# Kernel optimization log

Hardware: AMD Instinct MI355X
Metric: run time of the kernel (lower is better)

## Reference

```python
import jax, jax.numpy as jnp
import numpy as np

EMB_DIM = 256
ATTN_DIM = 64
N_HEADS = 2
B = 32768
K = 16


def setup_inputs() -> dict:
    key = jax.random.key(0)
    ks = jax.random.split(key, 8)
    center_emb = jax.random.normal(ks[0], (B, EMB_DIM), dtype=jnp.float32)
    neigh_embs = jax.random.normal(ks[1], (B, K, EMB_DIM), dtype=jnp.float32)
    neigh_weights = jax.random.uniform(ks[2], (B, K), dtype=jnp.float32)
    valid_mask = jax.random.randint(ks[3], (B,), 0, 2) > 0  # bool [B]
    # parameters (torch nn.Linear convention: y = x @ W.T)
    sq = 1.0 / np.sqrt(EMB_DIM)
    W_q = jax.random.uniform(ks[4], (N_HEADS, ATTN_DIM, EMB_DIM), minval=-sq, maxval=sq, dtype=jnp.float32)
    W_k = jax.random.uniform(ks[5], (N_HEADS, ATTN_DIM, EMB_DIM), minval=-sq, maxval=sq, dtype=jnp.float32)
    so = 1.0 / np.sqrt(EMB_DIM * N_HEADS)
    W_out = jax.random.uniform(ks[6], (EMB_DIM, EMB_DIM * N_HEADS), minval=-so, maxval=so, dtype=jnp.float32)
    b_out = jax.random.uniform(ks[7], (EMB_DIM,), minval=-so, maxval=so, dtype=jnp.float32)
    return {
        "center_emb": center_emb,
        "neigh_embs": neigh_embs,
        "neigh_weights": neigh_weights,
        "valid_mask": valid_mask,
        "W_q": W_q,
        "W_k": W_k,
        "W_out": W_out,
        "b_out": b_out,
    }


def reference(center_emb, neigh_embs, neigh_weights, valid_mask, W_q, W_k, W_out, b_out):
    # q: [B, H, A]; k: [B, H, K, A] (all heads vectorized)
    q = jnp.einsum("bd,had->bha", center_emb, W_q)
    k = jnp.einsum("bkd,had->bhka", neigh_embs, W_k)
    scores = jnp.einsum("bha,bhka->bhk", q, k) / jnp.sqrt(jnp.float32(ATTN_DIM))
    attn = jax.nn.softmax(scores, axis=-1) * neigh_weights[:, None, :]  # [B,H,K]
    attn = attn / (jnp.sum(attn, axis=-1, keepdims=True) + 1e-8)
    # dropout is identity in eval mode
    ctx = jnp.einsum("bhk,bkd->bhd", attn, neigh_embs)  # [B,H,D]
    multi_ctx = ctx.reshape(ctx.shape[0], -1)  # concat heads -> [B, H*D]
    out = multi_ctx @ W_out.T + b_out
    return jnp.where(valid_mask[:, None], out, center_emb)
```

## Files before the change

### kernel.cpp

```cpp
#include <hip/hip_runtime.h>
#include <hip/hip_bf16.h>

typedef unsigned short ushort_t;
typedef unsigned int uint32;

typedef __attribute__((ext_vector_type(8))) short bf16x8;
typedef __attribute__((ext_vector_type(4))) float f32x4;

__device__ __forceinline__ ushort_t f2bf(float f) {
    uint32 u = __float_as_uint(f);
    u += 0x7FFFu + ((u >> 16) & 1u);
    return (ushort_t)(u >> 16);
}
__device__ __forceinline__ float bf2f(ushort_t b) {
    return __uint_as_float(((uint32)b) << 16);
}

__global__ __launch_bounds__(256) void prep_kernel(
        const float* __restrict__ Wq, const float* __restrict__ Wk,
        const float* __restrict__ Wout,
        ushort_t* __restrict__ Mcomb, ushort_t* __restrict__ WoutB) {
    int idx = blockIdx.x * 256 + threadIdx.x;
    int n = idx >> 8;
    int e = idx & 255;
    int h = n >> 8;
    int d = n & 255;
    const float* wk = Wk + (h << 14);
    const float* wq = Wq + (h << 14);
    float acc = 0.f;
#pragma unroll 8
    for (int a = 0; a < 64; ++a) {
        acc += wk[(a << 8) + d] * wq[(a << 8) + e];
    }
    Mcomb[idx] = f2bf(acc * 0.125f);
    WoutB[idx] = f2bf(Wout[idx]);
}

#define LDT 72

__global__ __launch_bounds__(256) void gemm_qk(
        const float* __restrict__ A, const ushort_t* __restrict__ Bw,
        ushort_t* __restrict__ C) {
    __shared__ ushort_t As[64 * LDT];
    __shared__ ushort_t Bs[128 * LDT];
    const int t = threadIdx.x;
    const int m0 = blockIdx.x * 64;
    const int n0 = blockIdx.y * 128;
    const int lane = t & 63;
    const int w = t >> 6;
    const int wm = (w & 1) * 32;
    const int wn = (w >> 1) * 64;

    f32x4 zero = {0.f, 0.f, 0.f, 0.f};
    f32x4 acc[2][4];
#pragma unroll
    for (int i = 0; i < 2; ++i)
#pragma unroll
        for (int j = 0; j < 4; ++j) acc[i][j] = zero;

    for (int kc = 0; kc < 256; kc += 64) {
        __syncthreads();
#pragma unroll
        for (int i = 0; i < 4; ++i) {
            int f = i * 1024 + t * 4;
            int r = f >> 6;
            int c = f & 63;
            float4 v = *reinterpret_cast<const float4*>(&A[(size_t)(m0 + r) * 256 + kc + c]);
            ushort_t p[4] = {f2bf(v.x), f2bf(v.y), f2bf(v.z), f2bf(v.w)};
            *reinterpret_cast<uint2*>(&As[r * LDT + c]) = *reinterpret_cast<uint2*>(p);
        }
#pragma unroll
        for (int i = 0; i < 4; ++i) {
            int f = i * 2048 + t * 8;
            int r = f >> 6;
            int c = f & 63;
            uint4 v = *reinterpret_cast<const uint4*>(&Bw[(size_t)(n0 + r) * 256 + kc + c]);
            *reinterpret_cast<uint4*>(&Bs[r * LDT + c]) = v;
        }
        __syncthreads();
#pragma unroll
        for (int s = 0; s < 2; ++s) {
            int kb = s * 32 + (lane >> 4) * 8;
            bf16x8 af[2], bfr[4];
#pragma unroll
            for (int i = 0; i < 2; ++i)
                af[i] = *reinterpret_cast<const bf16x8*>(&As[(wm + i * 16 + (lane & 15)) * LDT + kb]);
#pragma unroll
            for (int j = 0; j < 4; ++j)
                bfr[j] = *reinterpret_cast<const bf16x8*>(&Bs[(wn + j * 16 + (lane & 15)) * LDT + kb]);
#pragma unroll
            for (int i = 0; i < 2; ++i)
#pragma unroll
                for (int j = 0; j < 4; ++j)
                    acc[i][j] = __builtin_amdgcn_mfma_f32_16x16x32_bf16(af[i], bfr[j], acc[i][j], 0, 0, 0);
        }
    }
    const int cn = lane & 15;
    const int r4 = (lane >> 4) * 4;
#pragma unroll
    for (int i = 0; i < 2; ++i)
#pragma unroll
        for (int j = 0; j < 4; ++j)
#pragma unroll
            for (int r = 0; r < 4; ++r) {
                int m = m0 + wm + i * 16 + r4 + r;
                int n = n0 + wn + j * 16 + cn;
                C[(size_t)m * 512 + n] = f2bf(acc[i][j][r]);
            }
}

#define XSS 264

__global__ __launch_bounds__(256) void attn_kernel(
        const float* __restrict__ neigh, const float* __restrict__ wts,
        const ushort_t* __restrict__ qk, ushort_t* __restrict__ ctx) {
    __shared__ ushort_t xs[4][16 * XSS];
    __shared__ float qs[4][512];
    __shared__ float at[4][32];
    const int t = threadIdx.x;
    const int w = t >> 6;
    const int lane = t & 63;
    const size_t b = (size_t)blockIdx.x * 4 + w;

    const float* xg = neigh + b * 4096;
#pragma unroll
    for (int k = 0; k < 16; ++k) {
        float4 v = *reinterpret_cast<const float4*>(&xg[k * 256 + lane * 4]);
        ushort_t p[4] = {f2bf(v.x), f2bf(v.y), f2bf(v.z), f2bf(v.w)};
        *reinterpret_cast<uint2*>(&xs[w][k * XSS + lane * 4]) = *reinterpret_cast<uint2*>(p);
    }
    {
        uint4 v = *reinterpret_cast<const uint4*>(&qk[b * 512 + lane * 8]);
        const ushort_t* xu = reinterpret_cast<const ushort_t*>(&v);
        float4 q0 = {bf2f(xu[0]), bf2f(xu[1]), bf2f(xu[2]), bf2f(xu[3])};
        float4 q1 = {bf2f(xu[4]), bf2f(xu[5]), bf2f(xu[6]), bf2f(xu[7])};
        *reinterpret_cast<float4*>(&qs[w][lane * 8]) = q0;
        *reinterpret_cast<float4*>(&qs[w][lane * 8 + 4]) = q1;
    }
    __syncthreads();

    const int p = lane & 31;
    const int half = lane >> 5;
    const int h = p >> 4;
    const int kn = p & 15;
    const ushort_t* xrow = &xs[w][kn * XSS + half * 128];
    const float* qrow = &qs[w][h * 256 + half * 128];
    float sc = 0.f;
#pragma unroll
    for (int j = 0; j < 16; ++j) {
        uint4 xv = *reinterpret_cast<const uint4*>(xrow + j * 8);
        const ushort_t* xu = reinterpret_cast<const ushort_t*>(&xv);
        float4 q0 = *reinterpret_cast<const float4*>(qrow + j * 8);
        float4 q1 = *reinterpret_cast<const float4*>(qrow + j * 8 + 4);
        sc += bf2f(xu[0]) * q0.x;
        sc += bf2f(xu[1]) * q0.y;
        sc += bf2f(xu[2]) * q0.z;
        sc += bf2f(xu[3]) * q0.w;
        sc += bf2f(xu[4]) * q1.x;
        sc += bf2f(xu[5]) * q1.y;
        sc += bf2f(xu[6]) * q1.z;
        sc += bf2f(xu[7]) * q1.w;
    }
    sc += __shfl_xor(sc, 32);

    float mx = sc;
#pragma unroll
    for (int m = 1; m < 16; m <<= 1) mx = fmaxf(mx, __shfl_xor(mx, m));
    float e = __expf(sc - mx);
    float se = e;
#pragma unroll
    for (int m = 1; m < 16; m <<= 1) se += __shfl_xor(se, m);
    float wv = wts[b * 16 + kn];
    float num = (e / se) * wv;
    float den = num;
#pragma unroll
    for (int m = 1; m < 16; m <<= 1) den += __shfl_xor(den, m);
    float attn = num / (den + 1e-8f);
    if (half == 0) at[w][h * 16 + kn] = attn;
    __syncthreads();

    const int h2 = lane >> 5;
    const int db = (lane & 31) * 8;
    float acc[8];
#pragma unroll
    for (int i = 0; i < 8; ++i) acc[i] = 0.f;
#pragma unroll
    for (int kk = 0; kk < 16; ++kk) {
        float a = at[w][h2 * 16 + kk];
        uint4 xv = *reinterpret_cast<const uint4*>(&xs[w][kk * XSS + db]);
        const ushort_t* xu = reinterpret_cast<const ushort_t*>(&xv);
#pragma unroll
        for (int i = 0; i < 8; ++i) acc[i] += a * bf2f(xu[i]);
    }
    ushort_t o[8];
#pragma unroll
    for (int i = 0; i < 8; ++i) o[i] = f2bf(acc[i]);
    *reinterpret_cast<uint4*>(&ctx[b * 512 + h2 * 256 + db]) = *reinterpret_cast<uint4*>(o);
}

__global__ __launch_bounds__(256) void gemm_out(
        const ushort_t* __restrict__ Abf, const ushort_t* __restrict__ Bw,
        const float* __restrict__ bias, const int* __restrict__ mask,
        const float* __restrict__ center, float* __restrict__ Out) {
    __shared__ ushort_t As[64 * LDT];
    __shared__ ushort_t Bs[128 * LDT];
    const int t = threadIdx.x;
    const int m0 = blockIdx.x * 64;
    const int n0 = blockIdx.y * 128;
    const int lane = t & 63;
    const int w = t >> 6;
    const int wm = (w & 1) * 32;
    const int wn = (w >> 1) * 64;

    f32x4 zero = {0.f, 0.f, 0.f, 0.f};
    f32x4 acc[2][4];
#pragma unroll
    for (int i = 0; i < 2; ++i)
#pragma unroll
        for (int j = 0; j < 4; ++j) acc[i][j] = zero;

    for (int kc = 0; kc < 512; kc += 64) {
        __syncthreads();
#pragma unroll
        for (int i = 0; i < 2; ++i) {
            int f = i * 2048 + t * 8;
            int r = f >> 6;
            int c = f & 63;
            uint4 v = *reinterpret_cast<const uint4*>(&Abf[(size_t)(m0 + r) * 512 + kc + c]);
            *reinterpret_cast<uint4*>(&As[r * LDT + c]) = v;
        }
#pragma unroll
        for (int i = 0; i < 4; ++i) {
            int f = i * 2048 + t * 8;
            int r = f >> 6;
            int c = f & 63;
            uint4 v = *reinterpret_cast<const uint4*>(&Bw[(size_t)(n0 + r) * 512 + kc + c]);
            *reinterpret_cast<uint4*>(&Bs[r * LDT + c]) = v;
        }
        __syncthreads();
#pragma unroll
        for (int s = 0; s < 2; ++s) {
            int kb = s * 32 + (lane >> 4) * 8;
            bf16x8 af[2], bfr[4];
#pragma unroll
            for (int i = 0; i < 2; ++i)
                af[i] = *reinterpret_cast<const bf16x8*>(&As[(wm + i * 16 + (lane & 15)) * LDT + kb]);
#pragma unroll
            for (int j = 0; j < 4; ++j)
                bfr[j] = *reinterpret_cast<const bf16x8*>(&Bs[(wn + j * 16 + (lane & 15)) * LDT + kb]);
#pragma unroll
            for (int i = 0; i < 2; ++i)
#pragma unroll
                for (int j = 0; j < 4; ++j)
                    acc[i][j] = __builtin_amdgcn_mfma_f32_16x16x32_bf16(af[i], bfr[j], acc[i][j], 0, 0, 0);
        }
    }
    const int cn = lane & 15;
    const int r4 = (lane >> 4) * 4;
#pragma unroll
    for (int i = 0; i < 2; ++i)
#pragma unroll
        for (int j = 0; j < 4; ++j)
#pragma unroll
            for (int r = 0; r < 4; ++r) {
                int m = m0 + wm + i * 16 + r4 + r;
                int n = n0 + wn + j * 16 + cn;
                float val = acc[i][j][r] + bias[n];
                float res = (mask[m] != 0) ? val : center[(size_t)m * 256 + n];
                Out[(size_t)m * 256 + n] = res;
            }
}

extern "C" void kernel_launch(void* const* d_in, const int* in_sizes, int n_in,
                              void* d_out, int out_size, void* d_ws, size_t ws_size,
                              hipStream_t stream) {
    const float* center = (const float*)d_in[0];
    const float* neigh  = (const float*)d_in[1];
    const float* wts    = (const float*)d_in[2];
    const int*   mask   = (const int*)d_in[3];
    const float* Wq     = (const float*)d_in[4];
    const float* Wk     = (const float*)d_in[5];
    const float* Wout   = (const float*)d_in[6];
    const float* bias   = (const float*)d_in[7];
    float* out = (float*)d_out;

    char* ws = (char*)d_ws;
    ushort_t* Mcomb  = (ushort_t*)(ws);
    ushort_t* WoutB  = (ushort_t*)(ws + (1 << 18));
    ushort_t* qkbuf  = (ushort_t*)(ws + (1 << 19));
    ushort_t* ctxbuf = (ushort_t*)(ws + (1 << 19) + (32u << 20));

    prep_kernel<<<512, 256, 0, stream>>>(Wq, Wk, Wout, Mcomb, WoutB);
    gemm_qk<<<dim3(512, 4), 256, 0, stream>>>(center, Mcomb, qkbuf);
    attn_kernel<<<8192, 256, 0, stream>>>(neigh, wts, qkbuf, ctxbuf);
    gemm_out<<<dim3(512, 2), 256, 0, stream>>>(ctxbuf, WoutB, bias, mask, center, out);
}
```

Before: 791.5 us.

## Skip masked rows in attention, widen output GEMM tile, stage QK stores

The attention kernel now reads the valid mask and skips loading neighbor embeddings and computing attention for rows whose output will be replaced by center_emb. This removes roughly half of the dominant neighbor-tensor read traffic, since the mask is random. The output GEMM now covers all 256 output columns per block, so the A tile is loaded once instead of twice, at the cost of more accumulators and LDS. The QK GEMM now stages its bf16 results through shared memory to emit coalesced 16-byte stores. Skipping masked rows is legitimate because those outputs are discarded by the reference, though the unwritten ctx rows are still read by the output GEMM (harmlessly discarded).

```diff
diff --git a/kernel.cpp b/kernel.cpp
--- a/kernel.cpp
+++ b/kernel.cpp
@@ -37,6 +37,7 @@
 }
 
 #define LDT 72
+#define CST 136
 
 __global__ __launch_bounds__(256) void gemm_qk(
         const float* __restrict__ A, const ushort_t* __restrict__ Bw,
@@ -95,6 +96,7 @@
                     acc[i][j] = __builtin_amdgcn_mfma_f32_16x16x32_bf16(af[i], bfr[j], acc[i][j], 0, 0, 0);
         }
     }
+    __syncthreads();
     const int cn = lane & 15;
     const int r4 = (lane >> 4) * 4;
 #pragma unroll
@@ -103,17 +105,26 @@
         for (int j = 0; j < 4; ++j)
 #pragma unroll
             for (int r = 0; r < 4; ++r) {
-                int m = m0 + wm + i * 16 + r4 + r;
-                int n = n0 + wn + j * 16 + cn;
-                C[(size_t)m * 512 + n] = f2bf(acc[i][j][r]);
+                int row = wm + i * 16 + r4 + r;
+                int col = wn + j * 16 + cn;
+                Bs[row * CST + col] = f2bf(acc[i][j][r]);
             }
+    __syncthreads();
+#pragma unroll
+    for (int it = 0; it < 4; ++it) {
+        int row = it * 16 + (t >> 4);
+        int cb = (t & 15) * 8;
+        uint4 v = *reinterpret_cast<const uint4*>(&Bs[row * CST + cb]);
+        *reinterpret_cast<uint4*>(&C[(size_t)(m0 + row) * 512 + n0 + cb]) = v;
+    }
 }
 
 #define XSS 264
 
 __global__ __launch_bounds__(256) void attn_kernel(
         const float* __restrict__ neigh, const float* __restrict__ wts,
-        const ushort_t* __restrict__ qk, ushort_t* __restrict__ ctx) {
+        const ushort_t* __restrict__ qk, const int* __restrict__ mask,
+        ushort_t* __restrict__ ctx) {
     __shared__ ushort_t xs[4][16 * XSS];
     __shared__ float qs[4][512];
     __shared__ float at[4][32];
@@ -121,15 +132,16 @@
     const int w = t >> 6;
     const int lane = t & 63;
     const size_t b = (size_t)blockIdx.x * 4 + w;
-
-    const float* xg = neigh + b * 4096;
-#pragma unroll
-    for (int k = 0; k < 16; ++k) {
-        float4 v = *reinterpret_cast<const float4*>(&xg[k * 256 + lane * 4]);
-        ushort_t p[4] = {f2bf(v.x), f2bf(v.y), f2bf(v.z), f2bf(v.w)};
-        *reinterpret_cast<uint2*>(&xs[w][k * XSS + lane * 4]) = *reinterpret_cast<uint2*>(p);
-    }
-    {
+    const bool active = (mask[b] != 0);
+
+    if (active) {
+        const float* xg = neigh + b * 4096;
+#pragma unroll
+        for (int k = 0; k < 16; ++k) {
+            float4 v = *reinterpret_cast<const float4*>(&xg[k * 256 + lane * 4]);
+            ushort_t p[4] = {f2bf(v.x), f2bf(v.y), f2bf(v.z), f2bf(v.w)};
+            *reinterpret_cast<uint2*>(&xs[w][k * XSS + lane * 4]) = *reinterpret_cast<uint2*>(p);
+        }
         uint4 v = *reinterpret_cast<const uint4*>(&qk[b * 512 + lane * 8]);
         const ushort_t* xu = reinterpret_cast<const ushort_t*>(&v);
         float4 q0 = {bf2f(xu[0]), bf2f(xu[1]), bf2f(xu[2]), bf2f(xu[3])};
@@ -139,63 +151,67 @@
     }
     __syncthreads();
 
-    const int p = lane & 31;
-    const int half = lane >> 5;
-    const int h = p >> 4;
-    const int kn = p & 15;
-    const ushort_t* xrow = &xs[w][kn * XSS + half * 128];
-    const float* qrow = &qs[w][h * 256 + half * 128];
-    float sc = 0.f;
-#pragma unroll
-    for (int j = 0; j < 16; ++j) {
-        uint4 xv = *reinterpret_cast<const uint4*>(xrow + j * 8);
-        const ushort_t* xu = reinterpret_cast<const ushort_t*>(&xv);
-        float4 q0 = *reinterpret_cast<const float4*>(qrow + j * 8);
-        float4 q1 = *reinterpret_cast<const float4*>(qrow + j * 8 + 4);
-        sc += bf2f(xu[0]) * q0.x;
-        sc += bf2f(xu[1]) * q0.y;
-        sc += bf2f(xu[2]) * q0.z;
-        sc += bf2f(xu[3]) * q0.w;
-        sc += bf2f(xu[4]) * q1.x;
-        sc += bf2f(xu[5]) * q1.y;
-        sc += bf2f(xu[6]) * q1.z;
-        sc += bf2f(xu[7]) * q1.w;
-    }
-    sc += __shfl_xor(sc, 32);
-
-    float mx = sc;
-#pragma unroll
-    for (int m = 1; m < 16; m <<= 1) mx = fmaxf(mx, __shfl_xor(mx, m));
-    float e = __expf(sc - mx);
-    float se = e;
-#pragma unroll
-    for (int m = 1; m < 16; m <<= 1) se += __shfl_xor(se, m);
-    float wv = wts[b * 16 + kn];
-    float num = (e / se) * wv;
-    float den = num;
-#pragma unroll
-    for (int m = 1; m < 16; m <<= 1) den += __shfl_xor(den, m);
-    float attn = num / (den + 1e-8f);
-    if (half == 0) at[w][h * 16 + kn] = attn;
+    if (active) {
+        const int p = lane & 31;
+        const int half = lane >> 5;
+        const int h = p >> 4;
+        const int kn = p & 15;
+        const ushort_t* xrow = &xs[w][kn * XSS + half * 128];
+        const float* qrow = &qs[w][h * 256 + half * 128];
+        float sc = 0.f;
+#pragma unroll
+        for (int j = 0; j < 16; ++j) {
+            uint4 xv = *reinterpret_cast<const uint4*>(xrow + j * 8);
+            const ushort_t* xu = reinterpret_cast<const ushort_t*>(&xv);
+            float4 q0 = *reinterpret_cast<const float4*>(qrow + j * 8);
+            float4 q1 = *reinterpret_cast<const float4*>(qrow + j * 8 + 4);
+            sc += bf2f(xu[0]) * q0.x;
+            sc += bf2f(xu[1]) * q0.y;
+            sc += bf2f(xu[2]) * q0.z;
+            sc += bf2f(xu[3]) * q0.w;
+            sc += bf2f(xu[4]) * q1.x;
+            sc += bf2f(xu[5]) * q1.y;
+            sc += bf2f(xu[6]) * q1.z;
+            sc += bf2f(xu[7]) * q1.w;
+        }
+        sc += __shfl_xor(sc, 32);
+
+        float mx = sc;
+#pragma unroll
+        for (int m = 1; m < 16; m <<= 1) mx = fmaxf(mx, __shfl_xor(mx, m));
+        float e = __expf(sc - mx);
+        float se = e;
+#pragma unroll
+        for (int m = 1; m < 16; m <<= 1) se += __shfl_xor(se, m);
+        float wv = wts[b * 16 + kn];
+        float num = (e / se) * wv;
+        float den = num;
+#pragma unroll
+        for (int m = 1; m < 16; m <<= 1) den += __shfl_xor(den, m);
+        float attn = num / (den + 1e-8f);
+        if (half == 0) at[w][h * 16 + kn] = attn;
+    }
     __syncthreads();
 
-    const int h2 = lane >> 5;
-    const int db = (lane & 31) * 8;
-    float acc[8];
-#pragma unroll
-    for (int i = 0; i < 8; ++i) acc[i] = 0.f;
-#pragma unroll
-    for (int kk = 0; kk < 16; ++kk) {
-        float a = at[w][h2 * 16 + kk];
-        uint4 xv = *reinterpret_cast<const uint4*>(&xs[w][kk * XSS + db]);
-        const ushort_t* xu = reinterpret_cast<const ushort_t*>(&xv);
-#pragma unroll
-        for (int i = 0; i < 8; ++i) acc[i] += a * bf2f(xu[i]);
-    }
-    ushort_t o[8];
-#pragma unroll
-    for (int i = 0; i < 8; ++i) o[i] = f2bf(acc[i]);
-    *reinterpret_cast<uint4*>(&ctx[b * 512 + h2 * 256 + db]) = *reinterpret_cast<uint4*>(o);
+    if (active) {
+        const int h2 = lane >> 5;
+        const int db = (lane & 31) * 8;
+        float acc[8];
+#pragma unroll
+        for (int i = 0; i < 8; ++i) acc[i] = 0.f;
+#pragma unroll
+        for (int kk = 0; kk < 16; ++kk) {
+            float a = at[w][h2 * 16 + kk];
+            uint4 xv = *reinterpret_cast<const uint4*>(&xs[w][kk * XSS + db]);
+            const ushort_t* xu = reinterpret_cast<const ushort_t*>(&xv);
+#pragma unroll
+            for (int i = 0; i < 8; ++i) acc[i] += a * bf2f(xu[i]);
+        }
+        ushort_t o[8];
+#pragma unroll
+        for (int i = 0; i < 8; ++i) o[i] = f2bf(acc[i]);
+        *reinterpret_cast<uint4*>(&ctx[b * 512 + h2 * 256 + db]) = *reinterpret_cast<uint4*>(o);
+    }
 }
 
 __global__ __launch_bounds__(256) void gemm_out(
@@ -203,21 +219,20 @@
         const float* __restrict__ bias, const int* __restrict__ mask,
         const float* __restrict__ center, float* __restrict__ Out) {
     __shared__ ushort_t As[64 * LDT];
-    __shared__ ushort_t Bs[128 * LDT];
+    __shared__ ushort_t Bs[256 * LDT];
     const int t = threadIdx.x;
     const int m0 = blockIdx.x * 64;
-    const int n0 = blockIdx.y * 128;
     const int lane = t & 63;
     const int w = t >> 6;
     const int wm = (w & 1) * 32;
-    const int wn = (w >> 1) * 64;
+    const int wn = (w >> 1) * 128;
 
     f32x4 zero = {0.f, 0.f, 0.f, 0.f};
-    f32x4 acc[2][4];
-#pragma unroll
-    for (int i = 0; i < 2; ++i)
-#pragma unroll
-        for (int j = 0; j < 4; ++j) acc[i][j] = zero;
+    f32x4 acc[2][8];
+#pragma unroll
+    for (int i = 0; i < 2; ++i)
+#pragma unroll
+        for (int j = 0; j < 8; ++j) acc[i][j] = zero;
 
     for (int kc = 0; kc < 512; kc += 64) {
         __syncthreads();
@@ -230,43 +245,49 @@
             *reinterpret_cast<uint4*>(&As[r * LDT + c]) = v;
         }
 #pragma unroll
-        for (int i = 0; i < 4; ++i) {
+        for (int i = 0; i < 8; ++i) {
             int f = i * 2048 + t * 8;
             int r = f >> 6;
             int c = f & 63;
-            uint4 v = *reinterpret_cast<const uint4*>(&Bw[(size_t)(n0 + r) * 512 + kc + c]);
+            uint4 v = *reinterpret_cast<const uint4*>(&Bw[(size_t)r * 512 + kc + c]);
             *reinterpret_cast<uint4*>(&Bs[r * LDT + c]) = v;
         }
         __syncthreads();
 #pragma unroll
         for (int s = 0; s < 2; ++s) {
             int kb = s * 32 + (lane >> 4) * 8;
-            bf16x8 af[2], bfr[4];
+            bf16x8 af[2], bfr[8];
 #pragma unroll
             for (int i = 0; i < 2; ++i)
                 af[i] = *reinterpret_cast<const bf16x8*>(&As[(wm + i * 16 + (lane & 15)) * LDT + kb]);
 #pragma unroll
-            for (int j = 0; j < 4; ++j)
+            for (int j = 0; j < 8; ++j)
                 bfr[j] = *reinterpret_cast<const bf16x8*>(&Bs[(wn + j * 16 + (lane & 15)) * LDT + kb]);
 #pragma unroll
             for (int i = 0; i < 2; ++i)
 #pragma unroll
-                for (int j = 0; j < 4; ++j)
+                for (int j = 0; j < 8; ++j)
                     acc[i][j] = __builtin_amdgcn_mfma_f32_16x16x32_bf16(af[i], bfr[j], acc[i][j], 0, 0, 0);
         }
     }
     const int cn = lane & 15;
     const int r4 = (lane >> 4) * 4;
-#pragma unroll
-    for (int i = 0; i < 2; ++i)
-#pragma unroll
-        for (int j = 0; j < 4; ++j)
+    int mk[2][4];
+#pragma unroll
+    for (int i = 0; i < 2; ++i)
+#pragma unroll
+        for (int r = 0; r < 4; ++r) mk[i][r] = mask[m0 + wm + i * 16 + r4 + r];
+#pragma unroll
+    for (int i = 0; i < 2; ++i)
+#pragma unroll
+        for (int j = 0; j < 8; ++j)
 #pragma unroll
             for (int r = 0; r < 4; ++r) {
                 int m = m0 + wm + i * 16 + r4 + r;
-                int n = n0 + wn + j * 16 + cn;
-                float val = acc[i][j][r] + bias[n];
-                float res = (mask[m] != 0) ? val : center[(size_t)m * 256 + n];
+                int n = wn + j * 16 + cn;
+                float res;
+                if (mk[i][r]) res = acc[i][j][r] + bias[n];
+                else          res = center[(size_t)m * 256 + n];
                 Out[(size_t)m * 256 + n] = res;
             }
 }
@@ -292,6 +313,6 @@
 
     prep_kernel<<<512, 256, 0, stream>>>(Wq, Wk, Wout, Mcomb, WoutB);
     gemm_qk<<<dim3(512, 4), 256, 0, stream>>>(center, Mcomb, qkbuf);
-    attn_kernel<<<8192, 256, 0, stream>>>(neigh, wts, qkbuf, ctxbuf);
-    gemm_out<<<dim3(512, 2), 256, 0, stream>>>(ctxbuf, WoutB, bias, mask, center, out);
-}
+    attn_kernel<<<8192, 256, 0, stream>>>(neigh, wts, qkbuf, mask, ctxbuf);
+    gemm_out<<<512, 256, 0, stream>>>(ctxbuf, WoutB, bias, mask, center, out);
+}
```

Measured after the change: 754.1 us. 4.7% less time.
